# Kernel optimization log

Hardware: AMD Instinct MI355X
Metric: run time of the kernel (lower is better)

## Reference

```python
import jax, jax.numpy as jnp
import numpy as np
import math

D = 1024
H = 16

def setup_inputs() -> dict:
    key = jax.random.key(0)
    ks = jax.random.split(key, 8)
    N, X, T = 2, 1024, 4096
    s = 1.0 / math.sqrt(D)
    return {
        "previous_output": jax.random.normal(ks[0], (N, X, D), jnp.float32),
        "context": jax.random.normal(ks[1], (N, T, D), jnp.float32),
        "Wq": jax.random.normal(ks[2], (D, D), jnp.float32) * s,
        "bq": jnp.zeros((D,), jnp.float32),
        "Wk": jax.random.normal(ks[3], (D, D), jnp.float32) * s,
        "bk": jnp.zeros((D,), jnp.float32),
        "Wv": jax.random.normal(ks[4], (D, D), jnp.float32) * s,
        "bv": jnp.zeros((D,), jnp.float32),
    }

def reference(previous_output, context, Wq, bq, Wk, bk, Wv, bv):
    N, X, _ = previous_output.shape
    T = context.shape[1]
    hd = D // H
    # linear projections (torch Linear: x @ W.T + b)
    q = (previous_output @ Wq.T + bq).reshape(N, X, H, hd).transpose(0, 2, 1, 3)  # (N,H,X,hd)
    k = (context @ Wk.T + bk).reshape(N, T, H, hd).transpose(0, 2, 1, 3)          # (N,H,T,hd)
    v = (context @ Wv.T + bv).reshape(N, T, H, hd).transpose(0, 2, 1, 3)          # (N,H,T,hd)
    scores = jnp.einsum('nhxd,nhtd->nhxt', q, k) / jnp.sqrt(jnp.float32(hd))       # (N,H,X,T)
    attn = jax.nn.softmax(scores, axis=-1)
    out = jnp.einsum('nhxt,nhtd->nhxd', attn, v)                                   # (N,H,X,hd)
    return out.transpose(0, 2, 1, 3).reshape(N, X, D)
```

## Files before the change

kernel.cpp:

```cpp
#include <hip/hip_runtime.h>

typedef __bf16 bf16_t;
typedef __bf16 bf16x8 __attribute__((ext_vector_type(8)));
typedef __bf16 bf16x4 __attribute__((ext_vector_type(4)));
typedef short short4v __attribute__((ext_vector_type(4)));
typedef float f32x4 __attribute__((ext_vector_type(4)));

#define D_MODEL 1024
#define NHEAD 16
#define HD 64
#define XLEN 1024
#define TLEN 4096
#define NBATCH 2
#define CEXP 0.18033688011112042f

typedef __attribute__((address_space(3))) bf16_t lds_bf16;
typedef const __attribute__((address_space(1))) bf16_t glb_bf16;

__global__ __launch_bounds__(256) void convert5(const float* __restrict__ prev, const float* __restrict__ ctx,
                                                const float* __restrict__ wq, const float* __restrict__ wk,
                                                const float* __restrict__ wv,
                                                bf16_t* __restrict__ prev_b, bf16_t* __restrict__ ctx_b,
                                                bf16_t* __restrict__ wq_b, bf16_t* __restrict__ wk_b,
                                                bf16_t* __restrict__ wv_b) {
    int b = blockIdx.x;
    const float* src; bf16_t* dst; int lb;
    if (b < 256)       { src = prev; dst = prev_b; lb = b; }
    else if (b < 1280) { src = ctx;  dst = ctx_b;  lb = b - 256; }
    else if (b < 1408) { src = wq;   dst = wq_b;   lb = b - 1280; }
    else if (b < 1536) { src = wk;   dst = wk_b;   lb = b - 1408; }
    else               { src = wv;   dst = wv_b;   lb = b - 1536; }
    const int base = lb * 8192 + threadIdx.x * 4;
#pragma unroll
    for (int i = 0; i < 8; ++i) {
        const int off = base + i * 1024;
        f32x4 f = *(const f32x4*)(src + off);
        bf16x4 h;
        h[0] = (bf16_t)f[0]; h[1] = (bf16_t)f[1]; h[2] = (bf16_t)f[2]; h[3] = (bf16_t)f[3];
        *(bf16x4*)(dst + off) = h;
    }
}

__global__ __launch_bounds__(256) void gemm_fused(const bf16_t* __restrict__ Xq, const bf16_t* __restrict__ Xc,
                                                  const bf16_t* __restrict__ wq, const bf16_t* __restrict__ wk,
                                                  const bf16_t* __restrict__ wv,
                                                  const float* __restrict__ bq, const float* __restrict__ bk,
                                                  const float* __restrict__ bv,
                                                  bf16_t* __restrict__ Qh, bf16_t* __restrict__ Kh,
                                                  bf16_t* __restrict__ Vt) {
    __shared__ bf16_t Ab[128][32];
    __shared__ bf16_t Bb[128][32];

    const int tid  = threadIdx.x;
    const int w    = tid >> 6;
    const int lane = tid & 63;
    const int q4   = lane >> 4;
    const int c    = lane & 15;

    const bf16_t* X; const bf16_t* W; const float* bias;
    int m0, n0, lshift, vmode;
    const int bid = blockIdx.x;
    if (bid < 128) {
        X = Xq; W = wq; bias = bq; lshift = 10; vmode = 0;
        m0 = (bid >> 3) * 128; n0 = (bid & 7) * 128;
    } else {
        const int b = bid - 128;
        const int xcd  = b & 7;
        const int s    = b >> 3;
        const int nb   = s >> 3;
        const int mgrp = s & 7;
        m0 = (mgrp * 8 + xcd) * 128;
        X = Xc; lshift = 12;
        if (nb < 8) { W = wk; bias = bk; vmode = 0; n0 = nb * 128; }
        else        { W = wv; bias = bv; vmode = 1; n0 = (nb - 8) * 128; }
    }

    f32x4 acc[4][4];
#pragma unroll
    for (int i = 0; i < 4; ++i)
#pragma unroll
        for (int j = 0; j < 4; ++j) acc[i][j] = (f32x4){0.f, 0.f, 0.f, 0.f};

    const int mq = (w & 1) * 64;
    const int nq = (w >> 1) * 64;

    bf16_t* aBase = &Ab[0][0] + w * 512;
    bf16_t* bBase = &Bb[0][0] + w * 512;
    const bf16_t* gA = X + (size_t)(m0 + (tid >> 2)) * D_MODEL + (tid & 3) * 8;
    const bf16_t* gB = W + (size_t)(n0 + (tid >> 2)) * D_MODEL + (tid & 3) * 8;

    for (int kk = 0; kk < D_MODEL; kk += 32) {
        __syncthreads();
        __builtin_amdgcn_global_load_lds((glb_bf16*)(gA + kk), (lds_bf16*)aBase, 16, 0, 0);
        __builtin_amdgcn_global_load_lds((glb_bf16*)(gA + kk + (size_t)64 * D_MODEL), (lds_bf16*)(aBase + 2048), 16, 0, 0);
        __builtin_amdgcn_global_load_lds((glb_bf16*)(gB + kk), (lds_bf16*)bBase, 16, 0, 0);
        __builtin_amdgcn_global_load_lds((glb_bf16*)(gB + kk + (size_t)64 * D_MODEL), (lds_bf16*)(bBase + 2048), 16, 0, 0);
        __syncthreads();

        bf16x8 a[4], b[4];
#pragma unroll
        for (int i = 0; i < 4; ++i) a[i] = *(const bf16x8*)&Ab[mq + i * 16 + c][q4 * 8];
#pragma unroll
        for (int i = 0; i < 4; ++i) b[i] = *(const bf16x8*)&Bb[nq + i * 16 + c][q4 * 8];
#pragma unroll
        for (int mi = 0; mi < 4; ++mi)
#pragma unroll
            for (int ni = 0; ni < 4; ++ni)
                acc[mi][ni] = __builtin_amdgcn_mfma_f32_16x16x32_bf16(a[mi], b[ni], acc[mi][ni], 0, 0, 0);
    }

    float bv4[4];
#pragma unroll
    for (int ni = 0; ni < 4; ++ni) bv4[ni] = bias[n0 + nq + ni * 16 + c];

    const int headbase = (n0 + nq) >> 6;
    if (vmode == 0) {
        bf16_t* OutQK = (bid < 128) ? Qh : Kh;
        const int L = 1 << lshift;
#pragma unroll
        for (int mi = 0; mi < 4; ++mi) {
            const int mrow = m0 + mq + mi * 16 + q4 * 4;
            const int nb2  = mrow >> lshift;
            const int pos  = mrow & (L - 1);
            bf16_t* ob = OutQK + ((size_t)(nb2 * NHEAD + headbase) * L + pos) * HD;
#pragma unroll
            for (int ni = 0; ni < 4; ++ni) {
                const int d = ni * 16 + c;
#pragma unroll
                for (int r = 0; r < 4; ++r)
                    ob[(size_t)r * HD + d] = (bf16_t)(acc[mi][ni][r] + bv4[ni]);
            }
        }
    } else {
#pragma unroll
        for (int mi = 0; mi < 4; ++mi) {
            const int mrow = m0 + mq + mi * 16 + q4 * 4;
            const int nb2  = mrow >> 12;
            const int pos  = mrow & 4095;
            const int lin  = (pos & ~31) + ((pos >> 2) & 3) * 8 + ((pos >> 4) & 1) * 4;
#pragma unroll
            for (int ni = 0; ni < 4; ++ni) {
                const int d = ni * 16 + c;
                bf16x4 v4;
#pragma unroll
                for (int r = 0; r < 4; ++r) v4[r] = (bf16_t)(acc[mi][ni][r] + bv4[ni]);
                *(bf16x4*)(Vt + ((size_t)(nb2 * NHEAD + headbase) * HD + d) * TLEN + lin) = v4;
            }
        }
    }
}

__global__ __launch_bounds__(256) void attn_kernel(const bf16_t* __restrict__ Qh,
                                                   const bf16_t* __restrict__ Kh,
                                                   const bf16_t* __restrict__ Vt,
                                                   bf16_t* __restrict__ Opart,
                                                   float* __restrict__ Lpart) {
    __shared__ bf16_t Kt[64 * 64];
    __shared__ bf16_t Vs[64 * 64];
    __shared__ bf16_t Ob[4][64][33];
    __shared__ float  Lb[4][32];

    const int tid  = threadIdx.x;
    const int lane = tid & 63;
    const int w    = tid >> 6;
    const int q4   = lane >> 4;
    const int c    = lane & 15;

    const int bid = blockIdx.x;
    const int xcd = bid & 7;
    const int seq = bid >> 3;
    const int tq  = seq & 3;
    const int xb  = (seq >> 2) & 7;
    const int g   = seq >> 5;
    const int nh  = g * 8 + xcd;
    const int xw  = xb * 128 + w * 32;

    const bf16_t* __restrict__ Kb = Kh + (size_t)nh * TLEN * HD;
    const bf16_t* __restrict__ Vb = Vt + (size_t)nh * HD * TLEN;

    bf16x8 qa[2][2];
#pragma unroll
    for (int mi = 0; mi < 2; ++mi) {
        const bf16_t* qr = Qh + ((size_t)nh * XLEN + xw + mi * 16 + c) * HD + q4 * 8;
        qa[mi][0] = *(const bf16x8*)(qr);
        qa[mi][1] = *(const bf16x8*)(qr + 32);
    }

    const int sRow0 = tid >> 3,   sRow1 = (256 + tid) >> 3;
    const int sCh   = tid & 7;
    const int kCol0 = ((sCh ^ (sRow0 & 7)) * 8);
    const int kCol1 = ((sCh ^ (sRow1 & 7)) * 8);
    bf16_t* ldsK0 = Kt + w * 512;
    bf16_t* ldsK1 = Kt + 2048 + w * 512;
    bf16_t* ldsV0 = Vs + w * 512;
    bf16_t* ldsV1 = Vs + 2048 + w * 512;

    int koff[2][2][2], voff[2][2][4];
#pragma unroll
    for (int g32 = 0; g32 < 2; ++g32) {
#pragma unroll
        for (int tt = 0; tt < 2; ++tt) {
#pragma unroll
            for (int dc = 0; dc < 2; ++dc)
                koff[g32][tt][dc] = (g32 * 32 + tt * 16 + c) * 128 + (((dc * 4 + q4 + 2) ^ (c & 7)) - 2 + ((dc * 4 + q4) ^ (c & 7)) - (((dc * 4 + q4 + 2) ^ (c & 7)) - 2)) * 16;
#pragma unroll
            for (int dt = 0; dt < 4; ++dt)
                voff[g32][tt][dt] = (dt * 16 + c) * 128 + (((g32 * 4 + q4) ^ (c & 7)) * 16) + tt * 8;
        }
    }
#pragma unroll
    for (int g32 = 0; g32 < 2; ++g32)
#pragma unroll
        for (int tt = 0; tt < 2; ++tt)
#pragma unroll
            for (int dc = 0; dc < 2; ++dc)
                koff[g32][tt][dc] = (g32 * 32 + tt * 16 + c) * 128 + (((dc * 4 + q4) ^ (c & 7)) * 16);

    f32x4 o[2][4];
#pragma unroll
    for (int i = 0; i < 2; ++i)
#pragma unroll
        for (int j = 0; j < 4; ++j) o[i][j] = (f32x4){0.f, 0.f, 0.f, 0.f};
    f32x4 lacc[2];
    lacc[0] = (f32x4){0.f, 0.f, 0.f, 0.f};
    lacc[1] = (f32x4){0.f, 0.f, 0.f, 0.f};

#if __has_builtin(__builtin_amdgcn_mfma_f32_16x16x16bf16_1k)
    bf16x4 ones4; ones4[0] = (bf16_t)1.0f; ones4[1] = (bf16_t)1.0f; ones4[2] = (bf16_t)1.0f; ones4[3] = (bf16_t)1.0f;
    const short4v onesS = __builtin_bit_cast(short4v, ones4);
#else
    bf16x8 ones8;
#pragma unroll
    for (int j = 0; j < 8; ++j) ones8[j] = (bf16_t)1.0f;
#endif

    const int t0base = tq * (TLEN / 4);
    for (int s = 0; s < 16; ++s) {
        const int t0 = t0base + s * 64;
        __syncthreads();
        __builtin_amdgcn_global_load_lds((glb_bf16*)(Kb + (size_t)(t0 + sRow0) * HD + kCol0), (lds_bf16*)ldsK0, 16, 0, 0);
        __builtin_amdgcn_global_load_lds((glb_bf16*)(Kb + (size_t)(t0 + sRow1) * HD + kCol1), (lds_bf16*)ldsK1, 16, 0, 0);
        __builtin_amdgcn_global_load_lds((glb_bf16*)(Vb + (size_t)sRow0 * TLEN + t0 + kCol0), (lds_bf16*)ldsV0, 16, 0, 0);
        __builtin_amdgcn_global_load_lds((glb_bf16*)(Vb + (size_t)sRow1 * TLEN + t0 + kCol1), (lds_bf16*)ldsV1, 16, 0, 0);
        __syncthreads();

#pragma unroll
        for (int g32 = 0; g32 < 2; ++g32) {
            bf16x4 pr[2][2];
#pragma unroll
            for (int tt = 0; tt < 2; ++tt) {
                bf16x8 kb0 = *(const bf16x8*)((const char*)Kt + koff[g32][tt][0]);
                bf16x8 kb1 = *(const bf16x8*)((const char*)Kt + koff[g32][tt][1]);
#pragma unroll
                for (int mi = 0; mi < 2; ++mi) {
                    f32x4 sv = (f32x4){0.f, 0.f, 0.f, 0.f};
                    sv = __builtin_amdgcn_mfma_f32_16x16x32_bf16(kb0, qa[mi][0], sv, 0, 0, 0);
                    sv = __builtin_amdgcn_mfma_f32_16x16x32_bf16(kb1, qa[mi][1], sv, 0, 0, 0);
                    bf16x4 p4;
#pragma unroll
                    for (int r = 0; r < 4; ++r) p4[r] = (bf16_t)__builtin_exp2f(sv[r] * CEXP);
                    pr[tt][mi] = p4;
                }
            }
#if __has_builtin(__builtin_amdgcn_mfma_f32_16x16x16bf16_1k)
#pragma unroll
            for (int mi = 0; mi < 2; ++mi)
#pragma unroll
                for (int tt = 0; tt < 2; ++tt) {
                    const short4v pb = __builtin_bit_cast(short4v, pr[tt][mi]);
#pragma unroll
                    for (int dt = 0; dt < 4; ++dt) {
                        bf16x4 va = *(const bf16x4*)((const char*)Vs + voff[g32][tt][dt]);
                        o[mi][dt] = __builtin_amdgcn_mfma_f32_16x16x16bf16_1k(
                            __builtin_bit_cast(short4v, va), pb, o[mi][dt], 0, 0, 0);
                    }
                    lacc[mi] = __builtin_amdgcn_mfma_f32_16x16x16bf16_1k(onesS, pb, lacc[mi], 0, 0, 0);
                }
#else
#pragma unroll
            for (int mi = 0; mi < 2; ++mi)
#pragma unroll
                for (int tt = 0; tt < 2; ++tt) {
                    bf16x8 p8;
#pragma unroll
                    for (int j = 0; j < 4; ++j) { p8[j] = pr[tt][mi][j]; p8[4 + j] = (bf16_t)0.0f; }
#pragma unroll
                    for (int dt = 0; dt < 4; ++dt) {
                        bf16x4 va = *(const bf16x4*)((const char*)Vs + voff[g32][tt][dt]);
                        bf16x8 va8;
#pragma unroll
                        for (int j = 0; j < 4; ++j) { va8[j] = va[j]; va8[4 + j] = (bf16_t)0.0f; }
                        o[mi][dt] = __builtin_amdgcn_mfma_f32_16x16x32_bf16(va8, p8, o[mi][dt], 0, 0, 0);
                    }
                    lacc[mi] = __builtin_amdgcn_mfma_f32_16x16x32_bf16(ones8, p8, lacc[mi], 0, 0, 0);
                }
#endif
        }
    }

#pragma unroll
    for (int mi = 0; mi < 2; ++mi) {
        if (q4 == 0) Lb[w][mi * 16 + c] = lacc[mi][0];
#pragma unroll
        for (int dt = 0; dt < 4; ++dt)
#pragma unroll
            for (int r = 0; r < 4; ++r)
                Ob[w][dt * 16 + q4 * 4 + r][mi * 16 + c] = (bf16_t)o[mi][dt][r];
    }
    {
        const int lr = lane >> 1;
        const int dh = lane & 1;
        bf16x8 out4[4];
#pragma unroll
        for (int j2 = 0; j2 < 4; ++j2)
#pragma unroll
            for (int e = 0; e < 8; ++e)
                out4[j2][e] = Ob[w][dh * 32 + j2 * 8 + e][lr];
        const size_t pair = (size_t)nh * XLEN + xw + lr;
        bf16_t* op = Opart + (pair * 4 + tq) * HD + dh * 32;
#pragma unroll
        for (int j2 = 0; j2 < 4; ++j2)
            *(bf16x8*)(op + j2 * 8) = out4[j2];
        if (dh == 0) Lpart[pair * 4 + tq] = Lb[w][lr];
    }
}

__global__ __launch_bounds__(256) void attn_merge(const bf16_t* __restrict__ Opart,
                                                  const float* __restrict__ Lpart,
                                                  float* __restrict__ Out) {
    const int u    = blockIdx.x * 256 + threadIdx.x;
    const int pair = u >> 3;
    const int d0   = (u & 7) * 8;
    const int nh   = pair >> 10;
    const int x    = pair & 1023;
    const int n    = nh >> 4;
    const int h    = nh & 15;

    float l = 0.f;
    float s[8];
#pragma unroll
    for (int j = 0; j < 8; ++j) s[j] = 0.f;
#pragma unroll
    for (int tqi = 0; tqi < 4; ++tqi) {
        l += Lpart[pair * 4 + tqi];
        bf16x8 v = *(const bf16x8*)(Opart + ((size_t)pair * 4 + tqi) * HD + d0);
#pragma unroll
        for (int j = 0; j < 8; ++j) s[j] += (float)v[j];
    }
    const float inv = 1.0f / l;
    f32x4 v0, v1;
#pragma unroll
    for (int j = 0; j < 4; ++j) { v0[j] = s[j] * inv; v1[j] = s[4 + j] * inv; }
    float* op = Out + ((size_t)(n * XLEN + x)) * D_MODEL + h * HD + d0;
    *(f32x4*)(op)     = v0;
    *(f32x4*)(op + 4) = v1;
}

extern "C" void kernel_launch(void* const* d_in, const int* in_sizes, int n_in,
                              void* d_out, int out_size, void* d_ws, size_t ws_size,
                              hipStream_t stream) {
    (void)in_sizes; (void)n_in; (void)out_size; (void)ws_size;
    const float* prev = (const float*)d_in[0];
    const float* ctx  = (const float*)d_in[1];
    const float* Wq   = (const float*)d_in[2];
    const float* bq   = (const float*)d_in[3];
    const float* Wk   = (const float*)d_in[4];
    const float* bk   = (const float*)d_in[5];
    const float* Wv   = (const float*)d_in[6];
    const float* bv   = (const float*)d_in[7];

    const size_t MiB = 1024 * 1024;
    char* ws = (char*)d_ws;
    bf16_t* prev_b = (bf16_t*)(ws);
    bf16_t* ctx_b  = (bf16_t*)(ws + 4 * MiB);
    bf16_t* wq_b   = (bf16_t*)(ws + 20 * MiB);
    bf16_t* wk_b   = (bf16_t*)(ws + 22 * MiB);
    bf16_t* wv_b   = (bf16_t*)(ws + 24 * MiB);
    bf16_t* Qh     = (bf16_t*)(ws + 26 * MiB);
    bf16_t* Kh     = (bf16_t*)(ws + 30 * MiB);
    bf16_t* Vt     = (bf16_t*)(ws + 46 * MiB);
    bf16_t* Opart  = ctx_b;
    float*  Lpart  = (float*)prev_b;

    convert5<<<1664, 256, 0, stream>>>(prev, ctx, Wq, Wk, Wv, prev_b, ctx_b, wq_b, wk_b, wv_b);
    gemm_fused<<<128 + 1024, 256, 0, stream>>>(prev_b, ctx_b, wq_b, wk_b, wv_b, bq, bk, bv, Qh, Kh, Vt);
    attn_kernel<<<1024, 256, 0, stream>>>(Qh, Kh, Vt, Opart, Lpart);
    attn_merge<<<1024, 256, 0, stream>>>(Opart, Lpart, (float*)d_out);
}
```

Before: 228.8 us.

## Halve attention query tile per wave, fold softmax scale into Q projection

Each attention wave now handles 16 query rows instead of 32, doubling the grid to 2048 blocks and setting launch bounds for 8 blocks per CU. The output staging buffer reuses the K/V shared memory, which cuts the LDS footprint. The exp2 scale constant moves into the Q projection epilogue, removing a multiply per score. In exchange, each K/V tile loaded into LDS is reused by half as many query rows, doubling K/V global traffic, while occupancy and latency hiding should improve.

```diff
diff --git a/kernel.cpp b/kernel.cpp
--- a/kernel.cpp
+++ b/kernel.cpp
@@ -74,6 +74,7 @@
         if (nb < 8) { W = wk; bias = bk; vmode = 0; n0 = nb * 128; }
         else        { W = wv; bias = bv; vmode = 1; n0 = (nb - 8) * 128; }
     }
+    const float osc = (bid < 128) ? CEXP : 1.0f;
 
     f32x4 acc[4][4];
 #pragma unroll
@@ -128,7 +129,7 @@
                 const int d = ni * 16 + c;
 #pragma unroll
                 for (int r = 0; r < 4; ++r)
-                    ob[(size_t)r * HD + d] = (bf16_t)(acc[mi][ni][r] + bv4[ni]);
+                    ob[(size_t)r * HD + d] = (bf16_t)((acc[mi][ni][r] + bv4[ni]) * osc);
             }
         }
     } else {
@@ -150,15 +151,15 @@
     }
 }
 
-__global__ __launch_bounds__(256) void attn_kernel(const bf16_t* __restrict__ Qh,
-                                                   const bf16_t* __restrict__ Kh,
-                                                   const bf16_t* __restrict__ Vt,
-                                                   bf16_t* __restrict__ Opart,
-                                                   float* __restrict__ Lpart) {
-    __shared__ bf16_t Kt[64 * 64];
-    __shared__ bf16_t Vs[64 * 64];
-    __shared__ bf16_t Ob[4][64][33];
-    __shared__ float  Lb[4][32];
+__global__ __launch_bounds__(256, 8) void attn_kernel(const bf16_t* __restrict__ Qh,
+                                                      const bf16_t* __restrict__ Kh,
+                                                      const bf16_t* __restrict__ Vt,
+                                                      bf16_t* __restrict__ Opart,
+                                                      float* __restrict__ Lpart) {
+    __shared__ __align__(16) char smem[16384 + 256];
+    bf16_t* Kt = (bf16_t*)smem;
+    bf16_t* Vs = Kt + 4096;
+    float*  Lb = (float*)(smem + 16384);
 
     const int tid  = threadIdx.x;
     const int lane = tid & 63;
@@ -170,23 +171,22 @@
     const int xcd = bid & 7;
     const int seq = bid >> 3;
     const int tq  = seq & 3;
-    const int xb  = (seq >> 2) & 7;
-    const int g   = seq >> 5;
+    const int xb  = (seq >> 2) & 15;
+    const int g   = seq >> 6;
     const int nh  = g * 8 + xcd;
-    const int xw  = xb * 128 + w * 32;
+    const int x0  = xb * 64 + w * 16;
 
     const bf16_t* __restrict__ Kb = Kh + (size_t)nh * TLEN * HD;
     const bf16_t* __restrict__ Vb = Vt + (size_t)nh * HD * TLEN;
 
-    bf16x8 qa[2][2];
-#pragma unroll
-    for (int mi = 0; mi < 2; ++mi) {
-        const bf16_t* qr = Qh + ((size_t)nh * XLEN + xw + mi * 16 + c) * HD + q4 * 8;
-        qa[mi][0] = *(const bf16x8*)(qr);
-        qa[mi][1] = *(const bf16x8*)(qr + 32);
-    }
-
-    const int sRow0 = tid >> 3,   sRow1 = (256 + tid) >> 3;
+    bf16x8 qa[2];
+    {
+        const bf16_t* qr = Qh + ((size_t)nh * XLEN + x0 + c) * HD + q4 * 8;
+        qa[0] = *(const bf16x8*)(qr);
+        qa[1] = *(const bf16x8*)(qr + 32);
+    }
+
+    const int sRow0 = tid >> 3,   sRow1 = 32 + (tid >> 3);
     const int sCh   = tid & 7;
     const int kCol0 = ((sCh ^ (sRow0 & 7)) * 8);
     const int kCol1 = ((sCh ^ (sRow1 & 7)) * 8);
@@ -195,35 +195,13 @@
     bf16_t* ldsV0 = Vs + w * 512;
     bf16_t* ldsV1 = Vs + 2048 + w * 512;
 
-    int koff[2][2][2], voff[2][2][4];
-#pragma unroll
-    for (int g32 = 0; g32 < 2; ++g32) {
-#pragma unroll
-        for (int tt = 0; tt < 2; ++tt) {
-#pragma unroll
-            for (int dc = 0; dc < 2; ++dc)
-                koff[g32][tt][dc] = (g32 * 32 + tt * 16 + c) * 128 + (((dc * 4 + q4 + 2) ^ (c & 7)) - 2 + ((dc * 4 + q4) ^ (c & 7)) - (((dc * 4 + q4 + 2) ^ (c & 7)) - 2)) * 16;
-#pragma unroll
-            for (int dt = 0; dt < 4; ++dt)
-                voff[g32][tt][dt] = (dt * 16 + c) * 128 + (((g32 * 4 + q4) ^ (c & 7)) * 16) + tt * 8;
-        }
-    }
-#pragma unroll
-    for (int g32 = 0; g32 < 2; ++g32)
-#pragma unroll
-        for (int tt = 0; tt < 2; ++tt)
-#pragma unroll
-            for (int dc = 0; dc < 2; ++dc)
-                koff[g32][tt][dc] = (g32 * 32 + tt * 16 + c) * 128 + (((dc * 4 + q4) ^ (c & 7)) * 16);
-
-    f32x4 o[2][4];
-#pragma unroll
-    for (int i = 0; i < 2; ++i)
-#pragma unroll
-        for (int j = 0; j < 4; ++j) o[i][j] = (f32x4){0.f, 0.f, 0.f, 0.f};
-    f32x4 lacc[2];
-    lacc[0] = (f32x4){0.f, 0.f, 0.f, 0.f};
-    lacc[1] = (f32x4){0.f, 0.f, 0.f, 0.f};
+    const int ofs0 = c * 128 + ((q4 ^ (c & 7)) * 16);
+    const int ofs1 = c * 128 + (((4 + q4) ^ (c & 7)) * 16);
+
+    f32x4 o[4];
+#pragma unroll
+    for (int j = 0; j < 4; ++j) o[j] = (f32x4){0.f, 0.f, 0.f, 0.f};
+    f32x4 lacc = (f32x4){0.f, 0.f, 0.f, 0.f};
 
 #if __has_builtin(__builtin_amdgcn_mfma_f32_16x16x16bf16_1k)
     bf16x4 ones4; ones4[0] = (bf16_t)1.0f; ones4[1] = (bf16_t)1.0f; ones4[2] = (bf16_t)1.0f; ones4[3] = (bf16_t)1.0f;
@@ -244,84 +222,75 @@
         __builtin_amdgcn_global_load_lds((glb_bf16*)(Vb + (size_t)sRow1 * TLEN + t0 + kCol1), (lds_bf16*)ldsV1, 16, 0, 0);
         __syncthreads();
 
+        const char* KtB = (const char*)Kt;
+        const char* VsB = (const char*)Vs;
 #pragma unroll
         for (int g32 = 0; g32 < 2; ++g32) {
-            bf16x4 pr[2][2];
+            bf16x4 pr[2];
 #pragma unroll
             for (int tt = 0; tt < 2; ++tt) {
-                bf16x8 kb0 = *(const bf16x8*)((const char*)Kt + koff[g32][tt][0]);
-                bf16x8 kb1 = *(const bf16x8*)((const char*)Kt + koff[g32][tt][1]);
-#pragma unroll
-                for (int mi = 0; mi < 2; ++mi) {
-                    f32x4 sv = (f32x4){0.f, 0.f, 0.f, 0.f};
-                    sv = __builtin_amdgcn_mfma_f32_16x16x32_bf16(kb0, qa[mi][0], sv, 0, 0, 0);
-                    sv = __builtin_amdgcn_mfma_f32_16x16x32_bf16(kb1, qa[mi][1], sv, 0, 0, 0);
-                    bf16x4 p4;
-#pragma unroll
-                    for (int r = 0; r < 4; ++r) p4[r] = (bf16_t)__builtin_exp2f(sv[r] * CEXP);
-                    pr[tt][mi] = p4;
+                const int rofs = g32 * 4096 + tt * 2048;
+                bf16x8 kb0 = *(const bf16x8*)(KtB + rofs + ofs0);
+                bf16x8 kb1 = *(const bf16x8*)(KtB + rofs + ofs1);
+                f32x4 sv = (f32x4){0.f, 0.f, 0.f, 0.f};
+                sv = __builtin_amdgcn_mfma_f32_16x16x32_bf16(kb0, qa[0], sv, 0, 0, 0);
+                sv = __builtin_amdgcn_mfma_f32_16x16x32_bf16(kb1, qa[1], sv, 0, 0, 0);
+                bf16x4 p4;
+#pragma unroll
+                for (int r = 0; r < 4; ++r) p4[r] = (bf16_t)__builtin_exp2f(sv[r]);
+                pr[tt] = p4;
+            }
+            const int vsel = g32 ? ofs1 : ofs0;
+#if __has_builtin(__builtin_amdgcn_mfma_f32_16x16x16bf16_1k)
+#pragma unroll
+            for (int tt = 0; tt < 2; ++tt) {
+                const short4v pb = __builtin_bit_cast(short4v, pr[tt]);
+#pragma unroll
+                for (int dt = 0; dt < 4; ++dt) {
+                    bf16x4 va = *(const bf16x4*)(VsB + vsel + dt * 2048 + tt * 8);
+                    o[dt] = __builtin_amdgcn_mfma_f32_16x16x16bf16_1k(
+                        __builtin_bit_cast(short4v, va), pb, o[dt], 0, 0, 0);
                 }
-            }
-#if __has_builtin(__builtin_amdgcn_mfma_f32_16x16x16bf16_1k)
-#pragma unroll
-            for (int mi = 0; mi < 2; ++mi)
-#pragma unroll
-                for (int tt = 0; tt < 2; ++tt) {
-                    const short4v pb = __builtin_bit_cast(short4v, pr[tt][mi]);
-#pragma unroll
-                    for (int dt = 0; dt < 4; ++dt) {
-                        bf16x4 va = *(const bf16x4*)((const char*)Vs + voff[g32][tt][dt]);
-                        o[mi][dt] = __builtin_amdgcn_mfma_f32_16x16x16bf16_1k(
-                            __builtin_bit_cast(short4v, va), pb, o[mi][dt], 0, 0, 0);
-                    }
-                    lacc[mi] = __builtin_amdgcn_mfma_f32_16x16x16bf16_1k(onesS, pb, lacc[mi], 0, 0, 0);
+                lacc = __builtin_amdgcn_mfma_f32_16x16x16bf16_1k(onesS, pb, lacc, 0, 0, 0);
+            }
+#else
+#pragma unroll
+            for (int tt = 0; tt < 2; ++tt) {
+                bf16x8 p8;
+#pragma unroll
+                for (int j = 0; j < 4; ++j) { p8[j] = pr[tt][j]; p8[4 + j] = (bf16_t)0.0f; }
+#pragma unroll
+                for (int dt = 0; dt < 4; ++dt) {
+                    bf16x4 va = *(const bf16x4*)(VsB + vsel + dt * 2048 + tt * 8);
+                    bf16x8 va8;
+#pragma unroll
+                    for (int j = 0; j < 4; ++j) { va8[j] = va[j]; va8[4 + j] = (bf16_t)0.0f; }
+                    o[dt] = __builtin_amdgcn_mfma_f32_16x16x32_bf16(va8, p8, o[dt], 0, 0, 0);
                 }
-#else
-#pragma unroll
-            for (int mi = 0; mi < 2; ++mi)
-#pragma unroll
-                for (int tt = 0; tt < 2; ++tt) {
-                    bf16x8 p8;
-#pragma unroll
-                    for (int j = 0; j < 4; ++j) { p8[j] = pr[tt][mi][j]; p8[4 + j] = (bf16_t)0.0f; }
-#pragma unroll
-                    for (int dt = 0; dt < 4; ++dt) {
-                        bf16x4 va = *(const bf16x4*)((const char*)Vs + voff[g32][tt][dt]);
-                        bf16x8 va8;
-#pragma unroll
-                        for (int j = 0; j < 4; ++j) { va8[j] = va[j]; va8[4 + j] = (bf16_t)0.0f; }
-                        o[mi][dt] = __builtin_amdgcn_mfma_f32_16x16x32_bf16(va8, p8, o[mi][dt], 0, 0, 0);
-                    }
-                    lacc[mi] = __builtin_amdgcn_mfma_f32_16x16x32_bf16(ones8, p8, lacc[mi], 0, 0, 0);
-                }
+                lacc = __builtin_amdgcn_mfma_f32_16x16x32_bf16(ones8, p8, lacc, 0, 0, 0);
+            }
 #endif
         }
     }
 
-#pragma unroll
-    for (int mi = 0; mi < 2; ++mi) {
-        if (q4 == 0) Lb[w][mi * 16 + c] = lacc[mi][0];
-#pragma unroll
-        for (int dt = 0; dt < 4; ++dt)
-#pragma unroll
-            for (int r = 0; r < 4; ++r)
-                Ob[w][dt * 16 + q4 * 4 + r][mi * 16 + c] = (bf16_t)o[mi][dt][r];
-    }
+    __syncthreads();
+    bf16_t* ObW = ((bf16_t*)smem) + w * 1152;
+    if (q4 == 0) Lb[w * 16 + c] = lacc[0];
+#pragma unroll
+    for (int dt = 0; dt < 4; ++dt)
+#pragma unroll
+        for (int r = 0; r < 4; ++r)
+            ObW[c * 72 + dt * 16 + q4 * 4 + r] = (bf16_t)o[dt][r];
     {
-        const int lr = lane >> 1;
-        const int dh = lane & 1;
-        bf16x8 out4[4];
-#pragma unroll
-        for (int j2 = 0; j2 < 4; ++j2)
-#pragma unroll
-            for (int e = 0; e < 8; ++e)
-                out4[j2][e] = Ob[w][dh * 32 + j2 * 8 + e][lr];
-        const size_t pair = (size_t)nh * XLEN + xw + lr;
-        bf16_t* op = Opart + (pair * 4 + tq) * HD + dh * 32;
-#pragma unroll
-        for (int j2 = 0; j2 < 4; ++j2)
-            *(bf16x8*)(op + j2 * 8) = out4[j2];
-        if (dh == 0) Lpart[pair * 4 + tq] = Lb[w][lr];
+        const int m  = lane >> 2;
+        const int dq = (lane & 3) * 16;
+        bf16x8 v0 = *(const bf16x8*)&ObW[m * 72 + dq];
+        bf16x8 v1 = *(const bf16x8*)&ObW[m * 72 + dq + 8];
+        const size_t pair = (size_t)nh * XLEN + x0 + m;
+        bf16_t* op = Opart + (pair * 4 + tq) * HD + dq;
+        *(bf16x8*)(op)     = v0;
+        *(bf16x8*)(op + 8) = v1;
+        if ((lane & 3) == 0) Lpart[pair * 4 + tq] = Lb[w * 16 + m];
     }
 }
 
@@ -384,6 +353,6 @@
 
     convert5<<<1664, 256, 0, stream>>>(prev, ctx, Wq, Wk, Wv, prev_b, ctx_b, wq_b, wk_b, wv_b);
     gemm_fused<<<128 + 1024, 256, 0, stream>>>(prev_b, ctx_b, wq_b, wk_b, wv_b, bq, bk, bv, Qh, Kh, Vt);
-    attn_kernel<<<1024, 256, 0, stream>>>(Qh, Kh, Vt, Opart, Lpart);
+    attn_kernel<<<2048, 256, 0, stream>>>(Qh, Kh, Vt, Opart, Lpart);
     attn_merge<<<1024, 256, 0, stream>>>(Opart, Lpart, (float*)d_out);
 }
```

New measurement: 243.1 us. 1.06x slower.

## Double-buffer K/V tiles in attention and fold softmax scale into Q

Applied to the files above, without the earlier changes.

The attention kernel now keeps two K/V tile buffers in LDS and prefetches the next tile while computing the current one, which removes the second barrier per iteration. The PV product switches from 16x16x16 MFMAs to 16x16x32 MFMAs with a single 8-wide probability operand, which reduces instruction count. The exp2 scale is folded into the Q projection epilogue, so the per-score multiply disappears. In exchange, LDS use doubles to 32KB per block, and launch bounds now request 4 blocks per CU.

```diff
diff --git a/kernel.cpp b/kernel.cpp
--- a/kernel.cpp
+++ b/kernel.cpp
@@ -3,7 +3,6 @@
 typedef __bf16 bf16_t;
 typedef __bf16 bf16x8 __attribute__((ext_vector_type(8)));
 typedef __bf16 bf16x4 __attribute__((ext_vector_type(4)));
-typedef short short4v __attribute__((ext_vector_type(4)));
 typedef float f32x4 __attribute__((ext_vector_type(4)));
 
 #define D_MODEL 1024
@@ -74,6 +73,7 @@
         if (nb < 8) { W = wk; bias = bk; vmode = 0; n0 = nb * 128; }
         else        { W = wv; bias = bv; vmode = 1; n0 = (nb - 8) * 128; }
     }
+    const float osc = (bid < 128) ? CEXP : 1.0f;
 
     f32x4 acc[4][4];
 #pragma unroll
@@ -128,7 +128,7 @@
                 const int d = ni * 16 + c;
 #pragma unroll
                 for (int r = 0; r < 4; ++r)
-                    ob[(size_t)r * HD + d] = (bf16_t)(acc[mi][ni][r] + bv4[ni]);
+                    ob[(size_t)r * HD + d] = (bf16_t)((acc[mi][ni][r] + bv4[ni]) * osc);
             }
         }
     } else {
@@ -150,15 +150,12 @@
     }
 }
 
-__global__ __launch_bounds__(256) void attn_kernel(const bf16_t* __restrict__ Qh,
-                                                   const bf16_t* __restrict__ Kh,
-                                                   const bf16_t* __restrict__ Vt,
-                                                   bf16_t* __restrict__ Opart,
-                                                   float* __restrict__ Lpart) {
-    __shared__ bf16_t Kt[64 * 64];
-    __shared__ bf16_t Vs[64 * 64];
-    __shared__ bf16_t Ob[4][64][33];
-    __shared__ float  Lb[4][32];
+__global__ __launch_bounds__(256, 4) void attn_kernel(const bf16_t* __restrict__ Qh,
+                                                      const bf16_t* __restrict__ Kh,
+                                                      const bf16_t* __restrict__ Vt,
+                                                      bf16_t* __restrict__ Opart,
+                                                      float* __restrict__ Lpart) {
+    __shared__ __align__(16) char smem[32768];
 
     const int tid  = threadIdx.x;
     const int lane = tid & 63;
@@ -186,35 +183,13 @@
         qa[mi][1] = *(const bf16x8*)(qr + 32);
     }
 
-    const int sRow0 = tid >> 3,   sRow1 = (256 + tid) >> 3;
+    const int sRow0 = tid >> 3,  sRow1 = 32 + (tid >> 3);
     const int sCh   = tid & 7;
     const int kCol0 = ((sCh ^ (sRow0 & 7)) * 8);
     const int kCol1 = ((sCh ^ (sRow1 & 7)) * 8);
-    bf16_t* ldsK0 = Kt + w * 512;
-    bf16_t* ldsK1 = Kt + 2048 + w * 512;
-    bf16_t* ldsV0 = Vs + w * 512;
-    bf16_t* ldsV1 = Vs + 2048 + w * 512;
-
-    int koff[2][2][2], voff[2][2][4];
-#pragma unroll
-    for (int g32 = 0; g32 < 2; ++g32) {
-#pragma unroll
-        for (int tt = 0; tt < 2; ++tt) {
-#pragma unroll
-            for (int dc = 0; dc < 2; ++dc)
-                koff[g32][tt][dc] = (g32 * 32 + tt * 16 + c) * 128 + (((dc * 4 + q4 + 2) ^ (c & 7)) - 2 + ((dc * 4 + q4) ^ (c & 7)) - (((dc * 4 + q4 + 2) ^ (c & 7)) - 2)) * 16;
-#pragma unroll
-            for (int dt = 0; dt < 4; ++dt)
-                voff[g32][tt][dt] = (dt * 16 + c) * 128 + (((g32 * 4 + q4) ^ (c & 7)) * 16) + tt * 8;
-        }
-    }
-#pragma unroll
-    for (int g32 = 0; g32 < 2; ++g32)
-#pragma unroll
-        for (int tt = 0; tt < 2; ++tt)
-#pragma unroll
-            for (int dc = 0; dc < 2; ++dc)
-                koff[g32][tt][dc] = (g32 * 32 + tt * 16 + c) * 128 + (((dc * 4 + q4) ^ (c & 7)) * 16);
+
+    const int ofs0 = c * 128 + ((q4 ^ (c & 7)) * 16);
+    const int ofs1 = c * 128 + (((4 + q4) ^ (c & 7)) * 16);
 
     f32x4 o[2][4];
 #pragma unroll
@@ -225,87 +200,77 @@
     lacc[0] = (f32x4){0.f, 0.f, 0.f, 0.f};
     lacc[1] = (f32x4){0.f, 0.f, 0.f, 0.f};
 
-#if __has_builtin(__builtin_amdgcn_mfma_f32_16x16x16bf16_1k)
-    bf16x4 ones4; ones4[0] = (bf16_t)1.0f; ones4[1] = (bf16_t)1.0f; ones4[2] = (bf16_t)1.0f; ones4[3] = (bf16_t)1.0f;
-    const short4v onesS = __builtin_bit_cast(short4v, ones4);
-#else
     bf16x8 ones8;
 #pragma unroll
     for (int j = 0; j < 8; ++j) ones8[j] = (bf16_t)1.0f;
-#endif
 
     const int t0base = tq * (TLEN / 4);
+
+    {
+        bf16_t* base = (bf16_t*)smem;
+        __builtin_amdgcn_global_load_lds((glb_bf16*)(Kb + (size_t)(t0base + sRow0) * HD + kCol0), (lds_bf16*)(base + w * 512), 16, 0, 0);
+        __builtin_amdgcn_global_load_lds((glb_bf16*)(Kb + (size_t)(t0base + sRow1) * HD + kCol1), (lds_bf16*)(base + 2048 + w * 512), 16, 0, 0);
+        __builtin_amdgcn_global_load_lds((glb_bf16*)(Vb + (size_t)sRow0 * TLEN + t0base + kCol0), (lds_bf16*)(base + 4096 + w * 512), 16, 0, 0);
+        __builtin_amdgcn_global_load_lds((glb_bf16*)(Vb + (size_t)sRow1 * TLEN + t0base + kCol1), (lds_bf16*)(base + 6144 + w * 512), 16, 0, 0);
+    }
+
     for (int s = 0; s < 16; ++s) {
-        const int t0 = t0base + s * 64;
         __syncthreads();
-        __builtin_amdgcn_global_load_lds((glb_bf16*)(Kb + (size_t)(t0 + sRow0) * HD + kCol0), (lds_bf16*)ldsK0, 16, 0, 0);
-        __builtin_amdgcn_global_load_lds((glb_bf16*)(Kb + (size_t)(t0 + sRow1) * HD + kCol1), (lds_bf16*)ldsK1, 16, 0, 0);
-        __builtin_amdgcn_global_load_lds((glb_bf16*)(Vb + (size_t)sRow0 * TLEN + t0 + kCol0), (lds_bf16*)ldsV0, 16, 0, 0);
-        __builtin_amdgcn_global_load_lds((glb_bf16*)(Vb + (size_t)sRow1 * TLEN + t0 + kCol1), (lds_bf16*)ldsV1, 16, 0, 0);
-        __syncthreads();
-
+        if (s < 15) {
+            const int t1 = t0base + (s + 1) * 64;
+            bf16_t* base = (bf16_t*)smem + ((s + 1) & 1) * 8192;
+            __builtin_amdgcn_global_load_lds((glb_bf16*)(Kb + (size_t)(t1 + sRow0) * HD + kCol0), (lds_bf16*)(base + w * 512), 16, 0, 0);
+            __builtin_amdgcn_global_load_lds((glb_bf16*)(Kb + (size_t)(t1 + sRow1) * HD + kCol1), (lds_bf16*)(base + 2048 + w * 512), 16, 0, 0);
+            __builtin_amdgcn_global_load_lds((glb_bf16*)(Vb + (size_t)sRow0 * TLEN + t1 + kCol0), (lds_bf16*)(base + 4096 + w * 512), 16, 0, 0);
+            __builtin_amdgcn_global_load_lds((glb_bf16*)(Vb + (size_t)sRow1 * TLEN + t1 + kCol1), (lds_bf16*)(base + 6144 + w * 512), 16, 0, 0);
+        }
+
+        const char* KtB = smem + (s & 1) * 16384;
+        const char* VsB = KtB + 8192;
 #pragma unroll
         for (int g32 = 0; g32 < 2; ++g32) {
-            bf16x4 pr[2][2];
+            bf16x8 p8[2];
 #pragma unroll
             for (int tt = 0; tt < 2; ++tt) {
-                bf16x8 kb0 = *(const bf16x8*)((const char*)Kt + koff[g32][tt][0]);
-                bf16x8 kb1 = *(const bf16x8*)((const char*)Kt + koff[g32][tt][1]);
+                const int rofs = g32 * 4096 + tt * 2048;
+                bf16x8 kb0 = *(const bf16x8*)(KtB + rofs + ofs0);
+                bf16x8 kb1 = *(const bf16x8*)(KtB + rofs + ofs1);
 #pragma unroll
                 for (int mi = 0; mi < 2; ++mi) {
                     f32x4 sv = (f32x4){0.f, 0.f, 0.f, 0.f};
                     sv = __builtin_amdgcn_mfma_f32_16x16x32_bf16(kb0, qa[mi][0], sv, 0, 0, 0);
                     sv = __builtin_amdgcn_mfma_f32_16x16x32_bf16(kb1, qa[mi][1], sv, 0, 0, 0);
-                    bf16x4 p4;
-#pragma unroll
-                    for (int r = 0; r < 4; ++r) p4[r] = (bf16_t)__builtin_exp2f(sv[r] * CEXP);
-                    pr[tt][mi] = p4;
+#pragma unroll
+                    for (int r = 0; r < 4; ++r)
+                        p8[mi][tt * 4 + r] = (bf16_t)__builtin_exp2f(sv[r]);
                 }
             }
-#if __has_builtin(__builtin_amdgcn_mfma_f32_16x16x16bf16_1k)
-#pragma unroll
-            for (int mi = 0; mi < 2; ++mi)
-#pragma unroll
-                for (int tt = 0; tt < 2; ++tt) {
-                    const short4v pb = __builtin_bit_cast(short4v, pr[tt][mi]);
-#pragma unroll
-                    for (int dt = 0; dt < 4; ++dt) {
-                        bf16x4 va = *(const bf16x4*)((const char*)Vs + voff[g32][tt][dt]);
-                        o[mi][dt] = __builtin_amdgcn_mfma_f32_16x16x16bf16_1k(
-                            __builtin_bit_cast(short4v, va), pb, o[mi][dt], 0, 0, 0);
-                    }
-                    lacc[mi] = __builtin_amdgcn_mfma_f32_16x16x16bf16_1k(onesS, pb, lacc[mi], 0, 0, 0);
-                }
-#else
-#pragma unroll
-            for (int mi = 0; mi < 2; ++mi)
-#pragma unroll
-                for (int tt = 0; tt < 2; ++tt) {
-                    bf16x8 p8;
-#pragma unroll
-                    for (int j = 0; j < 4; ++j) { p8[j] = pr[tt][mi][j]; p8[4 + j] = (bf16_t)0.0f; }
-#pragma unroll
-                    for (int dt = 0; dt < 4; ++dt) {
-                        bf16x4 va = *(const bf16x4*)((const char*)Vs + voff[g32][tt][dt]);
-                        bf16x8 va8;
-#pragma unroll
-                        for (int j = 0; j < 4; ++j) { va8[j] = va[j]; va8[4 + j] = (bf16_t)0.0f; }
-                        o[mi][dt] = __builtin_amdgcn_mfma_f32_16x16x32_bf16(va8, p8, o[mi][dt], 0, 0, 0);
-                    }
-                    lacc[mi] = __builtin_amdgcn_mfma_f32_16x16x32_bf16(ones8, p8, lacc[mi], 0, 0, 0);
-                }
-#endif
+            const int vsel = g32 ? ofs1 : ofs0;
+            bf16x8 va[4];
+#pragma unroll
+            for (int dt = 0; dt < 4; ++dt)
+                va[dt] = *(const bf16x8*)(VsB + vsel + dt * 2048);
+#pragma unroll
+            for (int mi = 0; mi < 2; ++mi) {
+#pragma unroll
+                for (int dt = 0; dt < 4; ++dt)
+                    o[mi][dt] = __builtin_amdgcn_mfma_f32_16x16x32_bf16(va[dt], p8[mi], o[mi][dt], 0, 0, 0);
+                lacc[mi] = __builtin_amdgcn_mfma_f32_16x16x32_bf16(ones8, p8[mi], lacc[mi], 0, 0, 0);
+            }
         }
     }
 
+    __syncthreads();
+    bf16_t* Ob = (bf16_t*)smem;
+    float*  Lb = (float*)(smem + 16896);
 #pragma unroll
     for (int mi = 0; mi < 2; ++mi) {
-        if (q4 == 0) Lb[w][mi * 16 + c] = lacc[mi][0];
+        if (q4 == 0) Lb[w * 32 + mi * 16 + c] = lacc[mi][0];
 #pragma unroll
         for (int dt = 0; dt < 4; ++dt)
 #pragma unroll
             for (int r = 0; r < 4; ++r)
-                Ob[w][dt * 16 + q4 * 4 + r][mi * 16 + c] = (bf16_t)o[mi][dt][r];
+                Ob[w * 2112 + (dt * 16 + q4 * 4 + r) * 33 + mi * 16 + c] = (bf16_t)o[mi][dt][r];
     }
     {
         const int lr = lane >> 1;
@@ -315,13 +280,13 @@
         for (int j2 = 0; j2 < 4; ++j2)
 #pragma unroll
             for (int e = 0; e < 8; ++e)
-                out4[j2][e] = Ob[w][dh * 32 + j2 * 8 + e][lr];
+                out4[j2][e] = Ob[w * 2112 + (dh * 32 + j2 * 8 + e) * 33 + lr];
         const size_t pair = (size_t)nh * XLEN + xw + lr;
         bf16_t* op = Opart + (pair * 4 + tq) * HD + dh * 32;
 #pragma unroll
         for (int j2 = 0; j2 < 4; ++j2)
             *(bf16x8*)(op + j2 * 8) = out4[j2];
-        if (dh == 0) Lpart[pair * 4 + tq] = Lb[w][lr];
+        if (dh == 0) Lpart[pair * 4 + tq] = Lb[w * 32 + lr];
     }
 }
 
```

Result: faster. 209.6 us (-8.4%).
